# Kernel tuning notes

Hardware: AMD Instinct MI355X
Metric: run time of the kernel (lower is better)

Reference implementation:

```python
import jax, jax.numpy as jnp
import numpy as np

GAMMA = 1.1
PC_MIN_XY, PC_MAX_XY = -75.2, 75.2


def setup_inputs() -> dict:
    key = jax.random.key(0)
    k1, k2, k3, k4, k5 = jax.random.split(key, 5)
    N, B, F = 200000, 256, 5
    # points: x,y in pc range, z in [-2,4], remaining features small
    xy = jax.random.uniform(k1, (N, 2), minval=PC_MIN_XY, maxval=PC_MAX_XY)
    z = jax.random.uniform(k2, (N, 1), minval=-2.0, maxval=4.0)
    feat = jax.random.normal(k3, (N, F - 3)) * 0.1
    cur_points = jnp.concatenate([xy, z, feat], axis=-1).astype(jnp.float32)
    # boxes: cx,cy,cz, dx,dy (sizes ~1..6 m), dz, heading
    centers = jax.random.uniform(k4, (B, 3), minval=PC_MIN_XY, maxval=PC_MAX_XY)
    sizes = jax.random.uniform(k5, (B, 3), minval=1.0, maxval=6.0)
    heading = jnp.zeros((B, 1), dtype=jnp.float32)
    cur_boxes = jnp.concatenate([centers, sizes, heading], axis=-1).astype(jnp.float32)
    return {"cur_points": cur_points, "cur_boxes": cur_boxes, "num_sample": 128}


def reference(cur_points, cur_boxes, num_sample):
    # cylindrical_pool: radius-mask + topk + gather (N >= num_sample, so no pad)
    # radii of cylinders: ||(dx,dy)/2|| * gamma  -> [B]
    cur_radiis = jnp.linalg.norm(cur_boxes[:, 3:5] * 0.5, axis=-1) * GAMMA
    # pairwise xy distance [B, N]
    dis = jnp.linalg.norm(cur_points[None, :, :2] - cur_boxes[:, None, :2], axis=-1)
    point_mask = (dis <= cur_radiis[:, None]).astype(cur_points.dtype)  # [B, N]
    # topk over 0/1 mask: in-radius points first (ties -> lowest index, like torch)
    sampled_mask, sampled_idx = jax.lax.top_k(point_mask, num_sample)  # [B, S]
    sampled_points = cur_points[sampled_idx]  # [B, S, F] gather
    sampled_points = jnp.where(sampled_mask[..., None] > 0, sampled_points, 0.0)
    return sampled_points
```

## Files before the change

kernel.cpp:

```cpp
#include <hip/hip_runtime.h>

#define GAMMA_F 1.1f
#define F_DIM 5
#define BOXG 8
#define MAX_NSEG 256

__device__ __forceinline__ int prefix_lt(unsigned long long m) {
  return __builtin_amdgcn_mbcnt_hi(
      (unsigned)(m >> 32), __builtin_amdgcn_mbcnt_lo((unsigned)m, 0u));
}

template <int NWAVE>
__global__ void __launch_bounds__(NWAVE * 64) seg_compact8_kernel(
    const float* __restrict__ pts, const float* __restrict__ boxes,
    int* __restrict__ cnt, unsigned short* __restrict__ idx, int N, int S,
    int NSEG, int L, int NGRP) {
  const int lane = threadIdx.x & 63;
  const int wid = threadIdx.x >> 6;
  const int g = blockIdx.x * NWAVE + wid;
  const int seg = g / NGRP;
  const int grp = g - seg * NGRP;
  const int box0 = grp * BOXG;

  float cx[BOXG], cy[BOXG], smax[BOXG];
#pragma unroll
  for (int b = 0; b < BOXG; ++b) {
    const float* bx = boxes + (box0 + b) * 7;
    cx[b] = bx[0];
    cy[b] = bx[1];
    const float hdx = __fmul_rn(bx[3], 0.5f);
    const float hdy = __fmul_rn(bx[4], 0.5f);
    const float r = __fmul_rn(
        __fsqrt_rn(__fadd_rn(__fmul_rn(hdx, hdx), __fmul_rn(hdy, hdy))),
        GAMMA_F);
    const unsigned ru = __float_as_uint(r);
    const float rsucc = __uint_as_float(ru + 1u);
    const double m = ((double)r + (double)rsucc) * 0.5;
    const double m2 = m * m;
    const bool incl = ((ru & 1u) == 0u);
    const float c1 = (float)m2;
    const double c1d = (double)c1;
    const bool keep = incl ? (c1d <= m2) : (c1d < m2);
    smax[b] = keep ? c1 : __uint_as_float(__float_as_uint(c1) - 1u);
  }

  const int start = seg * L;
  const int end = min(start + L, N);
  const int npts = end - start;

  int c[BOXG];
#pragma unroll
  for (int b = 0; b < BOXG; ++b) c[b] = 0;

  const size_t ibase = ((size_t)box0 * NSEG + seg) * S;
  const int nfull = (npts > 0) ? (npts / 128) : 0;

  const float* pp = pts + (size_t)(start + 2 * lane) * F_DIM;

#define PROCESS_8(RELBASE, X0, Y0, X1, Y1, G0, G1)                          \
  {                                                                         \
    const int rel = (RELBASE) + 2 * lane;                                   \
    _Pragma("unroll") for (int b = 0; b < BOXG; ++b) {                      \
      const float dx0 = __fsub_rn((X0), cx[b]);                             \
      const float dy0 = __fsub_rn((Y0), cy[b]);                             \
      const float s0 = __fadd_rn(__fmul_rn(dx0, dx0), __fmul_rn(dy0, dy0)); \
      const float dx1 = __fsub_rn((X1), cx[b]);                             \
      const float dy1 = __fsub_rn((Y1), cy[b]);                             \
      const float s1 = __fadd_rn(__fmul_rn(dx1, dx1), __fmul_rn(dy1, dy1)); \
      const bool sel0 = (G0) && (s0 <= smax[b]);                            \
      const bool sel1 = (G1) && (s1 <= smax[b]);                            \
      const unsigned long long m0 = __ballot(sel0);                         \
      const unsigned long long m1 = __ballot(sel1);                         \
      if (m0 | m1) {                                                        \
        const int p0 = prefix_lt(m0);                                       \
        const int p1 = prefix_lt(m1);                                       \
        const int r0 = c[b] + p0 + p1;                                      \
        const int r1 = c[b] + p0 + (sel0 ? 1 : 0) + p1;                     \
        unsigned short* mp = idx + ibase + (size_t)b * NSEG * S;            \
        if (sel0 && r0 < S) mp[r0] = (unsigned short)rel;                   \
        if (sel1 && r1 < S) mp[r1] = (unsigned short)(rel + 1);             \
        c[b] += __popcll(m0) + __popcll(m1);                                \
      }                                                                     \
    }                                                                       \
  }

  if (nfull > 0) {
    float x0 = pp[0], y0 = pp[1], x1 = pp[5], y1 = pp[6];
    for (int it = 0; it + 1 < nfull; ++it) {
      const float* pn = pp + 128 * F_DIM;
      const float nx0 = pn[0], ny0 = pn[1], nx1 = pn[5], ny1 = pn[6];
      PROCESS_8(it * 128, x0, y0, x1, y1, true, true);
      x0 = nx0;
      y0 = ny0;
      x1 = nx1;
      y1 = ny1;
      pp = pn;
    }
    PROCESS_8((nfull - 1) * 128, x0, y0, x1, y1, true, true);
    pp += 128 * F_DIM;
  }

  const int relb = nfull * 128;
  if (relb < npts) {
    const int rel = relb + 2 * lane;
    float x0 = 0.f, y0 = 0.f, x1 = 0.f, y1 = 0.f;
    const bool g0 = (rel < npts);
    const bool g1 = (rel + 1 < npts);
    if (g0) {
      x0 = pp[0];
      y0 = pp[1];
    }
    if (g1) {
      x1 = pp[5];
      y1 = pp[6];
    }
    PROCESS_8(relb, x0, y0, x1, y1, g0, g1);
  }
#undef PROCESS_8

  if (lane == 0) {
#pragma unroll
    for (int b = 0; b < BOXG; ++b) cnt[(box0 + b) * NSEG + seg] = min(c[b], S);
  }
}

__global__ void __launch_bounds__(256) gather_kernel(
    const float* __restrict__ pts, const int* __restrict__ cnt,
    const unsigned short* __restrict__ idx, float* __restrict__ out, int N,
    int S, int NSEG, int L) {
  const int b = blockIdx.x;
  const int tid = threadIdx.x;
  const int lane = tid & 63;
  const int wid = tid >> 6;

  __shared__ int pfx[MAX_NSEG + 1];
  __shared__ int wtot[4];
  __shared__ int woff[4];

  int v = (tid < NSEG) ? cnt[b * NSEG + tid] : 0;
  int sv = v;
#pragma unroll
  for (int d = 1; d < 64; d <<= 1) {
    const int t = __shfl_up(sv, d, 64);
    if (lane >= d) sv += t;
  }
  if (lane == 63) wtot[wid] = sv;
  __syncthreads();
  if (tid == 0) {
    int a = 0;
#pragma unroll
    for (int w = 0; w < 4; ++w) {
      woff[w] = a;
      a += wtot[w];
    }
  }
  __syncthreads();
  const int incl = sv + woff[wid];
  if (tid < NSEG) pfx[tid + 1] = incl;
  if (tid == 0) pfx[0] = 0;
  __syncthreads();

  const int total = pfx[NSEG];
  if (tid < S) {
    float* o = out + ((size_t)b * S + tid) * F_DIM;
    if (tid < total) {
      int lo = 0, hi = NSEG - 1;
      while (lo < hi) {
        const int mid = (lo + hi + 1) >> 1;
        if (pfx[mid] <= tid) lo = mid;
        else hi = mid - 1;
      }
      const int s = lo;
      const int gi =
          s * L + (int)idx[((size_t)b * NSEG + s) * S + (tid - pfx[s])];
      const float* p = pts + (size_t)gi * F_DIM;
      o[0] = p[0];
      o[1] = p[1];
      o[2] = p[2];
      o[3] = p[3];
      o[4] = p[4];
    } else {
      o[0] = 0.0f;
      o[1] = 0.0f;
      o[2] = 0.0f;
      o[3] = 0.0f;
      o[4] = 0.0f;
    }
  }
}

template <int BLOCK>
__global__ void __launch_bounds__(BLOCK) voxel_sampler_fallback(
    const float* __restrict__ pts, const float* __restrict__ boxes,
    float* __restrict__ out, int N, int S) {
  constexpr int NW = BLOCK / 64;
  const int b = blockIdx.x;
  const int tid = threadIdx.x;
  const int lane = tid & 63;
  const int wid = tid >> 6;

  const float cx = boxes[b * 7 + 0];
  const float cy = boxes[b * 7 + 1];
  const float hdx = __fmul_rn(boxes[b * 7 + 3], 0.5f);
  const float hdy = __fmul_rn(boxes[b * 7 + 4], 0.5f);
  const float r = __fmul_rn(
      __fsqrt_rn(__fadd_rn(__fmul_rn(hdx, hdx), __fmul_rn(hdy, hdy))),
      GAMMA_F);

  __shared__ int s_wsum[NW];
  __shared__ int s_count;
  if (tid == 0) s_count = 0;
  __syncthreads();

  float* outb = out + (size_t)b * S * F_DIM;

  for (int base = 0; base < N; base += BLOCK) {
    const int i = base + tid;
    bool sel = false;
    float x = 0.0f, y = 0.0f;
    if (i < N) {
      x = pts[i * F_DIM + 0];
      y = pts[i * F_DIM + 1];
      const float ddx = __fsub_rn(x, cx);
      const float ddy = __fsub_rn(y, cy);
      const float dis =
          __fsqrt_rn(__fadd_rn(__fmul_rn(ddx, ddx), __fmul_rn(ddy, ddy)));
      sel = (dis <= r);
    }
    const unsigned long long m = __ballot(sel);
    if (lane == 0) s_wsum[wid] = __popcll(m);
    __syncthreads();
    const int cbase = s_count;
    int wbase = 0;
    int tot = 0;
#pragma unroll
    for (int w = 0; w < NW; ++w) {
      const int v = s_wsum[w];
      if (w < wid) wbase += v;
      tot += v;
    }
    const int pos = cbase + wbase + __popcll(m & ((1ULL << lane) - 1ULL));
    if (sel && pos < S) {
      float* o = outb + pos * F_DIM;
      o[0] = x;
      o[1] = y;
      o[2] = pts[i * F_DIM + 2];
      o[3] = pts[i * F_DIM + 3];
      o[4] = pts[i * F_DIM + 4];
    }
    __syncthreads();
    if (tid == 0) s_count = cbase + tot;
    __syncthreads();
    if (cbase + tot >= S) break;
  }

  __syncthreads();
  int cnt = s_count;
  if (cnt > S) cnt = S;
  for (int j = cnt * F_DIM + tid; j < S * F_DIM; j += BLOCK) outb[j] = 0.0f;
}

extern "C" void kernel_launch(void* const* d_in, const int* in_sizes, int n_in,
                              void* d_out, int out_size, void* d_ws,
                              size_t ws_size, hipStream_t stream) {
  const float* pts = (const float*)d_in[0];
  const float* boxes = (const float*)d_in[1];
  float* out = (float*)d_out;

  const int N = in_sizes[0] / F_DIM;
  const int B = in_sizes[1] / 7;
  const int S = out_size / (B * F_DIM);

  const int NSEG = 256;
  int L = ((N + NSEG - 1) / NSEG + 1) & ~1;
  const int NGRP = B / BOXG;
  constexpr int NWAVE = 4;

  const size_t sz_cnt = (size_t)B * NSEG * sizeof(int);
  const size_t off_idx = (sz_cnt + 255) & ~(size_t)255;
  const size_t sz_idx = (size_t)B * NSEG * S * sizeof(unsigned short);
  const size_t need = off_idx + sz_idx;

  const bool fast = (ws_size >= need) && (L >= 2) && (L - 1 <= 65535) &&
                    (B % BOXG == 0) && (S <= 256) && (NSEG <= MAX_NSEG) &&
                    ((NSEG * NGRP) % NWAVE == 0) && (NWAVE <= NGRP) &&
                    ((size_t)L * NSEG >= (size_t)N);

  if (fast) {
    char* ws = (char*)d_ws;
    int* cnt = (int*)ws;
    unsigned short* idx = (unsigned short*)(ws + off_idx);

    seg_compact8_kernel<NWAVE>
        <<<(NSEG * NGRP) / NWAVE, NWAVE * 64, 0, stream>>>(
            pts, boxes, cnt, idx, N, S, NSEG, L, NGRP);
    gather_kernel<<<B, 256, 0, stream>>>(pts, cnt, idx, out, N, S, NSEG, L);
  } else {
    voxel_sampler_fallback<1024><<<B, 1024, 0, stream>>>(pts, boxes, out, N,
                                                         S);
  }
}
```

Measured before the change: 25.90 us.

## Stage segment point xy in LDS and share across box-group waves

Reorganizes the compaction kernel so each block owns one point segment and multiple box groups. The block cooperatively loads the segment's x,y coordinates into shared memory once, and each wave reads them as float4 pairs. Before, every wave re-read the strided point data from global memory. This adds a block barrier and LDS usage, doubles waves per block to 8, and requires L <= 1024 to take the fast path.

Measured after the change: 24.32 us. 1.06x faster.

```diff
diff --git a/kernel.cpp b/kernel.cpp
--- a/kernel.cpp
+++ b/kernel.cpp
@@ -4,6 +4,7 @@
 #define F_DIM 5
 #define BOXG 8
 #define MAX_NSEG 256
+#define MAXL 1024
 
 __device__ __forceinline__ int prefix_lt(unsigned long long m) {
   return __builtin_amdgcn_mbcnt_hi(
@@ -11,16 +12,24 @@
 }
 
 template <int NWAVE>
-__global__ void __launch_bounds__(NWAVE * 64) seg_compact8_kernel(
+__global__ void __launch_bounds__(NWAVE * 64, 4) seg_lds_kernel(
     const float* __restrict__ pts, const float* __restrict__ boxes,
     int* __restrict__ cnt, unsigned short* __restrict__ idx, int N, int S,
     int NSEG, int L, int NGRP) {
-  const int lane = threadIdx.x & 63;
-  const int wid = threadIdx.x >> 6;
-  const int g = blockIdx.x * NWAVE + wid;
-  const int seg = g / NGRP;
-  const int grp = g - seg * NGRP;
+  __shared__ __align__(16) float2 sxy[MAXL];
+
+  const int tid = threadIdx.x;
+  const int lane = tid & 63;
+  const int wid = tid >> 6;
+  const int bpg = NGRP / NWAVE;
+  const int seg = blockIdx.x / bpg;
+  const int bg = blockIdx.x - seg * bpg;
+  const int grp = bg * NWAVE + wid;
   const int box0 = grp * BOXG;
+
+  const int start = seg * L;
+  const int end = min(start + L, N);
+  const int npts = end - start;
 
   float cx[BOXG], cy[BOXG], smax[BOXG];
 #pragma unroll
@@ -44,18 +53,18 @@
     smax[b] = keep ? c1 : __uint_as_float(__float_as_uint(c1) - 1u);
   }
 
-  const int start = seg * L;
-  const int end = min(start + L, N);
-  const int npts = end - start;
+  for (int t = tid; t < npts; t += NWAVE * 64) {
+    const float* p = pts + (size_t)(start + t) * F_DIM;
+    sxy[t] = make_float2(p[0], p[1]);
+  }
+  __syncthreads();
 
   int c[BOXG];
 #pragma unroll
   for (int b = 0; b < BOXG; ++b) c[b] = 0;
 
   const size_t ibase = ((size_t)box0 * NSEG + seg) * S;
-  const int nfull = (npts > 0) ? (npts / 128) : 0;
-
-  const float* pp = pts + (size_t)(start + 2 * lane) * F_DIM;
+  const float4* sxy4 = (const float4*)sxy;
 
 #define PROCESS_8(RELBASE, X0, Y0, X1, Y1, G0, G1)                          \
   {                                                                         \
@@ -84,37 +93,18 @@
     }                                                                       \
   }
 
-  if (nfull > 0) {
-    float x0 = pp[0], y0 = pp[1], x1 = pp[5], y1 = pp[6];
-    for (int it = 0; it + 1 < nfull; ++it) {
-      const float* pn = pp + 128 * F_DIM;
-      const float nx0 = pn[0], ny0 = pn[1], nx1 = pn[5], ny1 = pn[6];
-      PROCESS_8(it * 128, x0, y0, x1, y1, true, true);
-      x0 = nx0;
-      y0 = ny0;
-      x1 = nx1;
-      y1 = ny1;
-      pp = pn;
-    }
-    PROCESS_8((nfull - 1) * 128, x0, y0, x1, y1, true, true);
-    pp += 128 * F_DIM;
-  }
-
+  const int nfull = npts / 128;
+  for (int it = 0; it < nfull; ++it) {
+    const float4 q = sxy4[it * 64 + lane];
+    PROCESS_8(it * 128, q.x, q.y, q.z, q.w, true, true);
+  }
   const int relb = nfull * 128;
   if (relb < npts) {
+    const float4 q = sxy4[nfull * 64 + lane];
     const int rel = relb + 2 * lane;
-    float x0 = 0.f, y0 = 0.f, x1 = 0.f, y1 = 0.f;
     const bool g0 = (rel < npts);
     const bool g1 = (rel + 1 < npts);
-    if (g0) {
-      x0 = pp[0];
-      y0 = pp[1];
-    }
-    if (g1) {
-      x1 = pp[5];
-      y1 = pp[6];
-    }
-    PROCESS_8(relb, x0, y0, x1, y1, g0, g1);
+    PROCESS_8(relb, q.x, q.y, q.z, q.w, g0, g1);
   }
 #undef PROCESS_8
 
@@ -274,16 +264,16 @@
   const int NSEG = 256;
   int L = ((N + NSEG - 1) / NSEG + 1) & ~1;
   const int NGRP = B / BOXG;
-  constexpr int NWAVE = 4;
+  constexpr int NWAVE = 8;
 
   const size_t sz_cnt = (size_t)B * NSEG * sizeof(int);
   const size_t off_idx = (sz_cnt + 255) & ~(size_t)255;
   const size_t sz_idx = (size_t)B * NSEG * S * sizeof(unsigned short);
   const size_t need = off_idx + sz_idx;
 
-  const bool fast = (ws_size >= need) && (L >= 2) && (L - 1 <= 65535) &&
-                    (B % BOXG == 0) && (S <= 256) && (NSEG <= MAX_NSEG) &&
-                    ((NSEG * NGRP) % NWAVE == 0) && (NWAVE <= NGRP) &&
+  const bool fast = (ws_size >= need) && (L >= 2) && (L <= MAXL) &&
+                    (L - 1 <= 65535) && (B % BOXG == 0) && (S <= 256) &&
+                    (NSEG <= MAX_NSEG) && (NGRP % NWAVE == 0) &&
                     ((size_t)L * NSEG >= (size_t)N);
 
   if (fast) {
@@ -291,9 +281,9 @@
     int* cnt = (int*)ws;
     unsigned short* idx = (unsigned short*)(ws + off_idx);
 
-    seg_compact8_kernel<NWAVE>
-        <<<(NSEG * NGRP) / NWAVE, NWAVE * 64, 0, stream>>>(
-            pts, boxes, cnt, idx, N, S, NSEG, L, NGRP);
+    const int bpg = NGRP / NWAVE;
+    seg_lds_kernel<NWAVE><<<NSEG * bpg, NWAVE * 64, 0, stream>>>(
+        pts, boxes, cnt, idx, N, S, NSEG, L, NGRP);
     gather_kernel<<<B, 256, 0, stream>>>(pts, cnt, idx, out, N, S, NSEG, L);
   } else {
     voxel_sampler_fallback<1024><<<B, 1024, 0, stream>>>(pts, boxes, out, N,
```
